# Performance work log

Measured on AMD Instinct MI355X. Metric: run time of the kernel, lower is better.

Reference implementation:

```python
import jax, jax.numpy as jnp
import numpy as np

D_MODEL = 1024
N_HEADS = 16
D_HEAD = D_MODEL // N_HEADS
B, L = 4, 2048


def setup_inputs() -> dict:
    key = jax.random.key(0)
    ks = jax.random.split(key, 10)
    s = 1.0 / np.sqrt(D_MODEL)
    inp = {
        "x": jax.random.normal(ks[0], (B, L, D_MODEL), dtype=jnp.float32),
        "src_key_padding_mask": jax.random.randint(ks[1], (B, L), 0, 2) > 0,
        "wq": jax.random.uniform(ks[2], (D_MODEL, D_MODEL), jnp.float32, -s, s),
        "bq": jnp.zeros((D_MODEL,), jnp.float32),
        "wk": jax.random.uniform(ks[3], (D_MODEL, D_MODEL), jnp.float32, -s, s),
        "bk": jnp.zeros((D_MODEL,), jnp.float32),
        "wv": jax.random.uniform(ks[4], (D_MODEL, D_MODEL), jnp.float32, -s, s),
        "bv": jnp.zeros((D_MODEL,), jnp.float32),
        "wo": jax.random.uniform(ks[5], (D_MODEL, D_MODEL), jnp.float32, -s, s),
        "bo": jnp.zeros((D_MODEL,), jnp.float32),
    }
    return inp


def reference(x, src_key_padding_mask, wq, bq, wk, bk, wv, bv, wo, bo):
    # dropout is identity in eval mode
    Bx, Lx, D = x.shape
    H, dh = N_HEADS, D_HEAD

    def proj(w, b):
        # torch nn.Linear: y = x @ w.T + b
        y = jnp.einsum('bld,ed->ble', x, w) + b
        return y.reshape(Bx, Lx, H, dh).transpose(0, 2, 1, 3)  # (B,H,L,dh)

    q = proj(wq, bq)
    k = proj(wk, bk)
    v = proj(wv, bv)

    scores = jnp.einsum('bhqd,bhkd->bhqk', q, k) / jnp.sqrt(jnp.float32(dh))
    scores = jnp.where(src_key_padding_mask[:, None, None, :], jnp.float32(-1e9), scores)
    attn = jax.nn.softmax(scores, axis=-1)
    out = jnp.einsum('bhqk,bhkd->bhqd', attn, v)
    out = out.transpose(0, 2, 1, 3).reshape(Bx, Lx, D)
    out = jnp.einsum('bld,ed->ble', out, wo) + bo
    return out
```

## Files before the change

### kernel.cpp

```cpp
#include <hip/hip_runtime.h>


typedef __attribute__((ext_vector_type(8))) short short8;
typedef __attribute__((ext_vector_type(4))) float f32x4;
typedef __attribute__((ext_vector_type(4))) float floatx4;
typedef __attribute__((ext_vector_type(4))) int int4v;
typedef __attribute__((ext_vector_type(2))) unsigned int u32x2;

#define MFMA16(a, b, c) __builtin_amdgcn_mfma_f32_16x16x32_bf16((a), (b), (c), 0, 0, 0)

__device__ __forceinline__ short f2bf(float f) {
    unsigned u = __float_as_uint(f);
    u += 0x7FFF + ((u >> 16) & 1);
    return (short)(u >> 16);
}

__global__ __launch_bounds__(256) void cvt_kernel(
    const float* __restrict__ src, short* __restrict__ dst, int n8)
{
    const int i = blockIdx.x * 256 + threadIdx.x;
    if (i >= n8) return;
    const f32x4* p = (const f32x4*)src + (size_t)i * 2;
    const f32x4 u0 = p[0];
    const f32x4 u1 = p[1];
    short8 s;
    s[0] = f2bf(u0[0]); s[1] = f2bf(u0[1]); s[2] = f2bf(u0[2]); s[3] = f2bf(u0[3]);
    s[4] = f2bf(u1[0]); s[5] = f2bf(u1[1]); s[6] = f2bf(u1[2]); s[7] = f2bf(u1[3]);
    ((short8*)dst)[i] = s;
}

__global__ __launch_bounds__(256, 2) void gemm_kernel(
    const short* __restrict__ A, const short* __restrict__ W,
    const float* __restrict__ bias, void* __restrict__ out, int layout)
{
    __shared__ short As[128 * 40];
    __shared__ short Bs[128 * 40];

    const int m0 = blockIdx.x * 128;
    const int n0 = blockIdx.y * 128;
    const int t = threadIdx.x;
    const int wave = t >> 6, lane = t & 63;
    const int wm = (wave >> 1) * 64, wn = (wave & 1) * 64;
    const int l15 = lane & 15, quad = lane >> 4;
    const int srow = t >> 2;
    const int scol = (t & 3) * 8;

    floatx4 acc[4][4];
#pragma unroll
    for (int i = 0; i < 4; i++)
#pragma unroll
        for (int j = 0; j < 4; j++) {
            acc[i][j][0] = 0.f; acc[i][j][1] = 0.f;
            acc[i][j][2] = 0.f; acc[i][j][3] = 0.f;
        }

    const size_t aoff0 = (size_t)(m0 + srow) * 1024 + scol;
    const size_t aoff1 = aoff0 + (size_t)64 * 1024;
    const size_t woff0 = (size_t)(n0 + srow) * 1024 + scol;
    const size_t woff1 = woff0 + (size_t)64 * 1024;

    short8 ra0 = *(const short8*)(A + aoff0);
    short8 ra1 = *(const short8*)(A + aoff1);
    short8 rb0 = *(const short8*)(W + woff0);
    short8 rb1 = *(const short8*)(W + woff1);

    for (int kb = 0; kb < 1024; kb += 32) {
        __syncthreads();
        *(short8*)&As[srow * 40 + scol]        = ra0;
        *(short8*)&As[(srow + 64) * 40 + scol] = ra1;
        *(short8*)&Bs[srow * 40 + scol]        = rb0;
        *(short8*)&Bs[(srow + 64) * 40 + scol] = rb1;
        __syncthreads();

        if (kb < 992) {
            ra0 = *(const short8*)(A + aoff0 + kb + 32);
            ra1 = *(const short8*)(A + aoff1 + kb + 32);
            rb0 = *(const short8*)(W + woff0 + kb + 32);
            rb1 = *(const short8*)(W + woff1 + kb + 32);
        }

        short8 af[4], bfr[4];
#pragma unroll
        for (int mi = 0; mi < 4; mi++)
            af[mi] = *(short8*)&As[(wm + mi * 16 + l15) * 40 + quad * 8];
#pragma unroll
        for (int ni = 0; ni < 4; ni++)
            bfr[ni] = *(short8*)&Bs[(wn + ni * 16 + l15) * 40 + quad * 8];
#pragma unroll
        for (int mi = 0; mi < 4; mi++)
#pragma unroll
            for (int ni = 0; ni < 4; ni++)
                acc[mi][ni] = MFMA16(af[mi], bfr[ni], acc[mi][ni]);
    }

#pragma unroll
    for (int ni = 0; ni < 4; ni++) {
        const int gn = n0 + wn + ni * 16 + l15;
        const float bv = bias[gn];
#pragma unroll
        for (int mi = 0; mi < 4; mi++) {
#pragma unroll
            for (int r = 0; r < 4; r++) {
                const int gm = m0 + wm + mi * 16 + quad * 4 + r;
                const float v = acc[mi][ni][r] + bv;
                if (layout == 3) {
                    ((float*)out)[(size_t)gm * 1024 + gn] = v;
                } else {
                    const int b = gm >> 11, l = gm & 2047;
                    const int h = gn >> 6,  d = gn & 63;
                    size_t idx;
                    if (layout == 2)
                        idx = ((size_t)(b * 16 + h) * 64 + d) * 2048 + l;
                    else
                        idx = ((size_t)(b * 16 + h) * 2048 + l) * 64 + d;
                    ((short*)out)[idx] = f2bf(v);
                }
            }
        }
    }
}

__global__ __launch_bounds__(256, 2) void attn_kernel(
    const short* __restrict__ Q, const short* __restrict__ Kc,
    const short* __restrict__ VT, const int* __restrict__ mask,
    float* __restrict__ O)
{
    __shared__ short Plds_all[4][4][16 * 72];

    const int blk = blockIdx.x;
    const int bh = blk & 63;
    const int qg = blk >> 6;
    const int b = bh >> 4, h = bh & 15;
    const int t = threadIdx.x;
    const int wave = t >> 6, lane = t & 63;
    const int l15 = lane & 15, quad = lane >> 4;

    const short* Qb = Q  + (size_t)bh * 2048 * 64;
    const short* Kb = Kc + (size_t)bh * 2048 * 64;
    const short* Vb = VT + (size_t)bh * 64 * 2048;
    const int* mrow = mask + b * 2048;

    const float SC = 0.125f * 1.44269504f;

    const int qbase = qg * 256 + wave * 64;

    short8 aq[4][2];
#pragma unroll
    for (int tt = 0; tt < 4; tt++) {
        const short* qp = Qb + (size_t)(qbase + tt * 16 + l15) * 64 + quad * 8;
        aq[tt][0] = *(const short8*)(qp);
        aq[tt][1] = *(const short8*)(qp + 32);
    }

    short8 vone;
#pragma unroll
    for (int j = 0; j < 8; j++) vone[j] = (short)0x3F80;

    floatx4 accO[4][5];
#pragma unroll
    for (int tt = 0; tt < 4; tt++)
#pragma unroll
        for (int ni = 0; ni < 5; ni++) {
            accO[tt][ni][0] = 0.f; accO[tt][ni][1] = 0.f;
            accO[tt][ni][2] = 0.f; accO[tt][ni][3] = 0.f;
        }

    for (int c0 = 0; c0 < 2048; c0 += 64) {
        short8 kreg[4][2];
#pragma unroll
        for (int g = 0; g < 4; g++) {
            const short* kp = Kb + (size_t)(c0 + g * 16 + l15) * 64 + quad * 8;
            kreg[g][0] = *(const short8*)(kp);
            kreg[g][1] = *(const short8*)(kp + 32);
        }
        f32x4 bias[4];
#pragma unroll
        for (int g = 0; g < 4; g++) {
            const int4v mv = *(const int4v*)&mrow[c0 + g * 16 + quad * 4];
#pragma unroll
            for (int r = 0; r < 4; r++) bias[g][r] = mv[r] ? -1e9f : 0.f;
        }
        short8 vreg[4][2];
#pragma unroll
        for (int ni = 0; ni < 4; ni++) {
            const short* vp = Vb + (size_t)(ni * 16 + l15) * 2048 + c0 + quad * 8;
            vreg[ni][0] = *(const short8*)(vp);
            vreg[ni][1] = *(const short8*)(vp + 32);
        }

#pragma unroll
        for (int tt = 0; tt < 4; tt++) {
            floatx4 s[4];
            __builtin_amdgcn_s_setprio(1);
#pragma unroll
            for (int g = 0; g < 4; g++) {
                floatx4 z = bias[g];
                z = MFMA16(kreg[g][0], aq[tt][0], z);
                s[g] = MFMA16(kreg[g][1], aq[tt][1], z);
            }
            __builtin_amdgcn_s_setprio(0);
            short* Pl = &Plds_all[wave][tt][0];
#pragma unroll
            for (int g = 0; g < 4; g++) {
                const float p0 = exp2f(s[g][0] * SC);
                const float p1 = exp2f(s[g][1] * SC);
                const float p2 = exp2f(s[g][2] * SC);
                const float p3 = exp2f(s[g][3] * SC);
                unsigned lo, hi;
                asm("v_cvt_pk_bf16_f32 %0, %1, %2" : "=v"(lo) : "v"(p0), "v"(p1));
                asm("v_cvt_pk_bf16_f32 %0, %1, %2" : "=v"(hi) : "v"(p2), "v"(p3));
                u32x2 w; w[0] = lo; w[1] = hi;
                *(u32x2*)&Pl[l15 * 72 + g * 16 + quad * 4] = w;
            }
        }

        asm volatile("s_waitcnt lgkmcnt(0)" ::: "memory");

#pragma unroll
        for (int tt = 0; tt < 4; tt++) {
            const short* Pl = &Plds_all[wave][tt][0];
            const short8 pa0 = *(const short8*)&Pl[l15 * 72 + quad * 8];
            const short8 pa1 = *(const short8*)&Pl[l15 * 72 + 32 + quad * 8];
            __builtin_amdgcn_s_setprio(1);
#pragma unroll
            for (int ni = 0; ni < 4; ni++) {
                accO[tt][ni] = MFMA16(pa0, vreg[ni][0], accO[tt][ni]);
                accO[tt][ni] = MFMA16(pa1, vreg[ni][1], accO[tt][ni]);
            }
            accO[tt][4] = MFMA16(pa0, vone, accO[tt][4]);
            accO[tt][4] = MFMA16(pa1, vone, accO[tt][4]);
            __builtin_amdgcn_s_setprio(0);
        }
    }

#pragma unroll
    for (int tt = 0; tt < 4; tt++) {
#pragma unroll
        for (int r = 0; r < 4; r++) {
            const float inv = 1.0f / fmaxf(accO[tt][4][r], 1e-30f);
            const int l = qbase + tt * 16 + quad * 4 + r;
#pragma unroll
            for (int ni = 0; ni < 4; ni++) {
                O[(size_t)(b * 2048 + l) * 1024 + h * 64 + ni * 16 + l15] =
                    accO[tt][ni][r] * inv;
            }
        }
    }
}

extern "C" void kernel_launch(void* const* d_in, const int* in_sizes, int n_in,
                              void* d_out, int out_size, void* d_ws, size_t ws_size,
                              hipStream_t stream)
{
    const float* x    = (const float*)d_in[0];
    const int*   mask = (const int*)d_in[1];
    const float* wq   = (const float*)d_in[2];
    const float* bq   = (const float*)d_in[3];
    const float* wk   = (const float*)d_in[4];
    const float* bk   = (const float*)d_in[5];
    const float* wv   = (const float*)d_in[6];
    const float* bv   = (const float*)d_in[7];
    const float* wo   = (const float*)d_in[8];
    const float* bo   = (const float*)d_in[9];
    float* out = (float*)d_out;

    short* Qbuf = (short*)d_ws;
    short* Kbuf = Qbuf + (size_t)8 * 1024 * 1024;
    short* Vt   = Kbuf + (size_t)8 * 1024 * 1024;

    short* Xb  = (short*)d_out;
    short* Wqb = Xb  + (size_t)8 * 1024 * 1024;
    short* Wkb = Wqb + (size_t)1024 * 1024;
    short* Wvb = Wkb + (size_t)1024 * 1024;

    dim3 block(256);

    cvt_kernel<<<dim3(4096), block, 0, stream>>>(x,  Xb,  1024 * 1024);
    cvt_kernel<<<dim3(512),  block, 0, stream>>>(wq, Wqb, 128 * 1024);
    cvt_kernel<<<dim3(512),  block, 0, stream>>>(wk, Wkb, 128 * 1024);
    cvt_kernel<<<dim3(512),  block, 0, stream>>>(wv, Wvb, 128 * 1024);

    dim3 grid(64, 8);
    gemm_kernel<<<grid, block, 0, stream>>>(Xb, Wqb, bq, Qbuf, 0);
    gemm_kernel<<<grid, block, 0, stream>>>(Xb, Wkb, bk, Kbuf, 1);
    gemm_kernel<<<grid, block, 0, stream>>>(Xb, Wvb, bv, Vt, 2);

    attn_kernel<<<dim3(512), block, 0, stream>>>(Qbuf, Kbuf, Vt, mask, out);

    short* Ob  = Qbuf;
    short* Wob = Kbuf;
    cvt_kernel<<<dim3(4096), block, 0, stream>>>(out, Ob,  1024 * 1024);
    cvt_kernel<<<dim3(512),  block, 0, stream>>>(wo,  Wob, 128 * 1024);

    gemm_kernel<<<grid, block, 0, stream>>>(Ob, Wob, bo, out, 3);
}
```

Baseline: 377.7 us.

## Fuse QKV GEMMs and conversions, load GEMM tiles directly into LDS

```diff
diff --git a/kernel.cpp b/kernel.cpp
--- a/kernel.cpp
+++ b/kernel.cpp
@@ -15,11 +15,14 @@
     return (short)(u >> 16);
 }
 
-__global__ __launch_bounds__(256) void cvt_kernel(
-    const float* __restrict__ src, short* __restrict__ dst, int n8)
-{
-    const int i = blockIdx.x * 256 + threadIdx.x;
-    if (i >= n8) return;
+__device__ __forceinline__ void gload_lds16(const short* g, short* l) {
+    __builtin_amdgcn_global_load_lds(
+        (const __attribute__((address_space(1))) void*)g,
+        (__attribute__((address_space(3))) void*)l, 16, 0, 0);
+}
+
+__device__ __forceinline__ void cvt8(const float* __restrict__ src,
+                                     short* __restrict__ dst, int i) {
     const f32x4* p = (const f32x4*)src + (size_t)i * 2;
     const f32x4 u0 = p[0];
     const f32x4 u1 = p[1];
@@ -29,21 +32,62 @@
     ((short8*)dst)[i] = s;
 }
 
-__global__ __launch_bounds__(256, 2) void gemm_kernel(
+__global__ __launch_bounds__(256) void cvt_kernel(
+    const float* __restrict__ src, short* __restrict__ dst, int n8)
+{
+    const int i = blockIdx.x * 256 + threadIdx.x;
+    if (i >= n8) return;
+    cvt8(src, dst, i);
+}
+
+__global__ __launch_bounds__(256) void cvt3_kernel(
+    const float* __restrict__ s0, const float* __restrict__ s1,
+    const float* __restrict__ s2, short* __restrict__ d0,
+    short* __restrict__ d1, short* __restrict__ d2)
+{
+    const int which = blockIdx.x >> 9;
+    const int i = (blockIdx.x & 511) * 256 + threadIdx.x;
+    const float* s = which == 0 ? s0 : which == 1 ? s1 : s2;
+    short* d = which == 0 ? d0 : which == 1 ? d1 : d2;
+    cvt8(s, d, i);
+}
+
+__global__ __launch_bounds__(256) void cvt2_kernel(
+    const float* __restrict__ s0, short* __restrict__ d0,
+    const float* __restrict__ s1, short* __restrict__ d1)
+{
+    if (blockIdx.x < 4096) {
+        cvt8(s0, d0, blockIdx.x * 256 + threadIdx.x);
+    } else {
+        cvt8(s1, d1, (blockIdx.x - 4096) * 256 + threadIdx.x);
+    }
+}
+
+__device__ __forceinline__ void gemm_body(
     const short* __restrict__ A, const short* __restrict__ W,
-    const float* __restrict__ bias, void* __restrict__ out, int layout)
-{
-    __shared__ short As[128 * 40];
-    __shared__ short Bs[128 * 40];
-
-    const int m0 = blockIdx.x * 128;
-    const int n0 = blockIdx.y * 128;
+    const float* __restrict__ bias, void* __restrict__ out,
+    int layout, int m0, int n0)
+{
+    __shared__ short As[128 * 32];
+    __shared__ short Bs[128 * 32];
+
     const int t = threadIdx.x;
     const int wave = t >> 6, lane = t & 63;
     const int wm = (wave >> 1) * 64, wn = (wave & 1) * 64;
     const int l15 = lane & 15, quad = lane >> 4;
-    const int srow = t >> 2;
-    const int scol = (t & 3) * 8;
+
+    const int r4 = lane >> 2;
+    const int kc = (lane & 3) * 8;
+
+    short* lA0 = &As[wave * 512 + lane * 8];
+    short* lA1 = &As[2048 + wave * 512 + lane * 8];
+    short* lB0 = &Bs[wave * 512 + lane * 8];
+    short* lB1 = &Bs[2048 + wave * 512 + lane * 8];
+
+    const short* gA0 = A + (size_t)(m0 + wave * 16 + r4) * 1024 + kc;
+    const short* gA1 = gA0 + (size_t)64 * 1024;
+    const short* gB0 = W + (size_t)(n0 + wave * 16 + r4) * 1024 + kc;
+    const short* gB1 = gB0 + (size_t)64 * 1024;
 
     floatx4 acc[4][4];
 #pragma unroll
@@ -54,43 +98,27 @@
             acc[i][j][2] = 0.f; acc[i][j][3] = 0.f;
         }
 
-    const size_t aoff0 = (size_t)(m0 + srow) * 1024 + scol;
-    const size_t aoff1 = aoff0 + (size_t)64 * 1024;
-    const size_t woff0 = (size_t)(n0 + srow) * 1024 + scol;
-    const size_t woff1 = woff0 + (size_t)64 * 1024;
-
-    short8 ra0 = *(const short8*)(A + aoff0);
-    short8 ra1 = *(const short8*)(A + aoff1);
-    short8 rb0 = *(const short8*)(W + woff0);
-    short8 rb1 = *(const short8*)(W + woff1);
-
     for (int kb = 0; kb < 1024; kb += 32) {
+        gload_lds16(gA0 + kb, lA0);
+        gload_lds16(gA1 + kb, lA1);
+        gload_lds16(gB0 + kb, lB0);
+        gload_lds16(gB1 + kb, lB1);
         __syncthreads();
-        *(short8*)&As[srow * 40 + scol]        = ra0;
-        *(short8*)&As[(srow + 64) * 40 + scol] = ra1;
-        *(short8*)&Bs[srow * 40 + scol]        = rb0;
-        *(short8*)&Bs[(srow + 64) * 40 + scol] = rb1;
-        __syncthreads();
-
-        if (kb < 992) {
-            ra0 = *(const short8*)(A + aoff0 + kb + 32);
-            ra1 = *(const short8*)(A + aoff1 + kb + 32);
-            rb0 = *(const short8*)(W + woff0 + kb + 32);
-            rb1 = *(const short8*)(W + woff1 + kb + 32);
-        }
 
         short8 af[4], bfr[4];
 #pragma unroll
         for (int mi = 0; mi < 4; mi++)
-            af[mi] = *(short8*)&As[(wm + mi * 16 + l15) * 40 + quad * 8];
+            af[mi] = *(short8*)&As[(wm + mi * 16 + l15) * 32 + quad * 8];
 #pragma unroll
         for (int ni = 0; ni < 4; ni++)
-            bfr[ni] = *(short8*)&Bs[(wn + ni * 16 + l15) * 40 + quad * 8];
+            bfr[ni] = *(short8*)&Bs[(wn + ni * 16 + l15) * 32 + quad * 8];
 #pragma unroll
         for (int mi = 0; mi < 4; mi++)
 #pragma unroll
             for (int ni = 0; ni < 4; ni++)
                 acc[mi][ni] = MFMA16(af[mi], bfr[ni], acc[mi][ni]);
+
+        __syncthreads();
     }
 
 #pragma unroll
@@ -120,6 +148,29 @@
     }
 }
 
+__global__ __launch_bounds__(256, 3) void qkv_kernel(
+    const short* __restrict__ Xb,
+    const short* __restrict__ Wq, const short* __restrict__ Wk,
+    const short* __restrict__ Wv,
+    const float* __restrict__ bq, const float* __restrict__ bk,
+    const float* __restrict__ bv,
+    short* __restrict__ Qo, short* __restrict__ Ko, short* __restrict__ Vo)
+{
+    const int chunk = blockIdx.y >> 3;
+    const int n0 = (blockIdx.y & 7) * 128;
+    const short* W = chunk == 0 ? Wq : chunk == 1 ? Wk : Wv;
+    const float* bs = chunk == 0 ? bq : chunk == 1 ? bk : bv;
+    void* out = chunk == 0 ? (void*)Qo : chunk == 1 ? (void*)Ko : (void*)Vo;
+    gemm_body(Xb, W, bs, out, chunk, blockIdx.x * 128, n0);
+}
+
+__global__ __launch_bounds__(256, 3) void gemm_kernel(
+    const short* __restrict__ A, const short* __restrict__ W,
+    const float* __restrict__ bias, void* __restrict__ out, int layout)
+{
+    gemm_body(A, W, bias, out, layout, blockIdx.x * 128, blockIdx.y * 128);
+}
+
 __global__ __launch_bounds__(256, 2) void attn_kernel(
     const short* __restrict__ Q, const short* __restrict__ Kc,
     const short* __restrict__ VT, const int* __restrict__ mask,
@@ -275,22 +326,17 @@
 
     dim3 block(256);
 
-    cvt_kernel<<<dim3(4096), block, 0, stream>>>(x,  Xb,  1024 * 1024);
-    cvt_kernel<<<dim3(512),  block, 0, stream>>>(wq, Wqb, 128 * 1024);
-    cvt_kernel<<<dim3(512),  block, 0, stream>>>(wk, Wkb, 128 * 1024);
-    cvt_kernel<<<dim3(512),  block, 0, stream>>>(wv, Wvb, 128 * 1024);
-
-    dim3 grid(64, 8);
-    gemm_kernel<<<grid, block, 0, stream>>>(Xb, Wqb, bq, Qbuf, 0);
-    gemm_kernel<<<grid, block, 0, stream>>>(Xb, Wkb, bk, Kbuf, 1);
-    gemm_kernel<<<grid, block, 0, stream>>>(Xb, Wvb, bv, Vt, 2);
+    cvt_kernel<<<dim3(4096), block, 0, stream>>>(x, Xb, 1024 * 1024);
+    cvt3_kernel<<<dim3(1536), block, 0, stream>>>(wq, wk, wv, Wqb, Wkb, Wvb);
+
+    qkv_kernel<<<dim3(64, 24), block, 0, stream>>>(
+        Xb, Wqb, Wkb, Wvb, bq, bk, bv, Qbuf, Kbuf, Vt);
 
     attn_kernel<<<dim3(512), block, 0, stream>>>(Qbuf, Kbuf, Vt, mask, out);
 
     short* Ob  = Qbuf;
     short* Wob = Kbuf;
-    cvt_kernel<<<dim3(4096), block, 0, stream>>>(out, Ob,  1024 * 1024);
-    cvt_kernel<<<dim3(512),  block, 0, stream>>>(wo,  Wob, 128 * 1024);
-
-    gemm_kernel<<<grid, block, 0, stream>>>(Ob, Wob, bo, out, 3);
-}
+    cvt2_kernel<<<dim3(4608), block, 0, stream>>>(out, Ob, wo, Wob);
+
+    gemm_kernel<<<dim3(64, 8), block, 0, stream>>>(Ob, Wob, bo, out, 3);
+}
```

After: 357.4 us. -5.4%, faster.
